# Kernel tuning notes

Hardware: AMD Instinct MI355X
Metric: run time of the kernel (lower is better)

Reference implementation:

```python
import jax, jax.numpy as jnp
import numpy as np
from jax import lax

B, FCH, H, W = 2, 48, 512, 512
WNUM, PATCH = 1, 8
DEG = 180.0 / np.pi
# well-conditioned, slightly asymmetric fallback Mueller matrix for masked (non-physical) pixels
_SAFE = np.array([[1.0, 0.02, 0.01, 0.005],
                  [0.0, 0.95, 0.05, 0.0],
                  [0.0, -0.05, 0.90, 0.04],
                  [0.0, 0.0, -0.04, 0.85]], dtype=np.float32)


def setup_inputs():
    key = jax.random.key(0)
    x = 0.5 * jax.random.normal(key, (B, FCH, H, W), dtype=jnp.float32)
    eye = jnp.eye(4, dtype=jnp.float32).reshape(16)
    # bias intensity frames and both calibration matrices toward 2*I so per-pixel
    # 4x4 systems are well conditioned and M is near-physical
    boost = jnp.concatenate([2.0 * eye, 2.0 * eye, 2.0 * eye])[None, :, None, None]
    return {"x": x + boost}


def _charpoly_mask(M):
    # Cloude realizability test: characteristic-polynomial coefficients of the
    # Hermitian coherency matrix must all be >= 0 (all eigenvalues >= 0).
    s = jnp.stack([jnp.eye(2, dtype=jnp.complex64),
                   jnp.array([[1, 0], [0, -1]], jnp.complex64),
                   jnp.array([[0, 1], [1, 0]], jnp.complex64),
                   jnp.array([[0, -1j], [1j, 0]], jnp.complex64)])
    Bk = jnp.einsum('iab,jcd->ijacbd', s, s).reshape(16, 4, 4)  # kron(sigma_i, sigma_j)
    Hc = 0.25 * jnp.einsum('...k,kab->...ab', M.reshape(M.shape[:-2] + (16,)).astype(jnp.complex64), Bk)
    tr1 = jnp.trace(Hc, axis1=-2, axis2=-1).real
    H2 = Hc @ Hc
    tr2 = jnp.trace(H2, axis1=-2, axis2=-1).real
    tr3 = jnp.trace(H2 @ Hc, axis1=-2, axis2=-1).real
    c2 = 0.5 * (tr1 ** 2 - tr2)
    c3 = (tr1 ** 3 - 3.0 * tr1 * tr2 + 2.0 * tr3) / 6.0
    c4 = jnp.linalg.det(Hc).real
    return (tr1 >= 0) & (c2 >= 0) & (c3 >= 0) & (c4 >= 0)


def _compute_mm(A, F, Wm, norm=True):
    M = jnp.linalg.solve(A, F)  # A^-1 F
    M = jnp.swapaxes(jnp.linalg.solve(jnp.swapaxes(Wm, -1, -2), jnp.swapaxes(M, -1, -2)), -1, -2)  # ... W^-1
    return M / M[..., 0:1, 0:1] if norm else M


def _lu_chipman(M, mask):
    # Lu-Chipman polar decomposition M = M_delta @ M_R @ M_D (per pixel)
    M = jnp.where(mask[..., None, None], M, jnp.asarray(_SAFE))
    I3 = jnp.eye(3, dtype=M.dtype)
    D = M[..., 0, 1:]  # diattenuation vector
    d2 = jnp.clip(jnp.sum(D * D, -1), 0.0, 1.0 - 1e-6)
    d = jnp.sqrt(d2 + 1e-12)
    sq = jnp.sqrt(1.0 - d2)
    Dh = D / jnp.maximum(d, 1e-6)[..., None]
    mD = sq[..., None, None] * I3 + (1.0 - sq)[..., None, None] * (Dh[..., :, None] * Dh[..., None, :])
    ones = jnp.ones(M.shape[:-2] + (1,), M.dtype)
    MD = jnp.concatenate([jnp.concatenate([ones, D], -1)[..., None, :],
                          jnp.concatenate([D[..., None], mD], -1)], -2)
    Mp = jnp.swapaxes(jnp.linalg.solve(MD, jnp.swapaxes(M, -1, -2)), -1, -2)  # M @ MD^-1 (MD symmetric)
    mp = Mp[..., 1:, 1:]
    mm = mp @ jnp.swapaxes(mp, -1, -2)
    lam = jnp.clip(jnp.linalg.eigvalsh(mm), 1e-12, None)  # ascending
    s1, s2, s3 = jnp.sqrt(lam[..., 2]), jnp.sqrt(lam[..., 1]), jnp.sqrt(lam[..., 0])
    sgn = jnp.where(jnp.linalg.det(mp) < 0, -1.0, 1.0).astype(M.dtype)
    A3 = mm + (s1 * s2 + s2 * s3 + s3 * s1)[..., None, None] * I3 + 1e-6 * I3
    B3 = (s1 + s2 + s3)[..., None, None] * mm + (s1 * s2 * s3)[..., None, None] * I3
    mdel = sgn[..., None, None] * jnp.linalg.solve(A3, B3)
    Pdel = (M[..., 1:, 0] - jnp.einsum('...ij,...j->...i', M[..., 1:, 1:], D)) / (1.0 - d2)[..., None]
    top = jnp.concatenate([ones, jnp.zeros(M.shape[:-2] + (3,), M.dtype)], -1)[..., None, :]
    Mdel = jnp.concatenate([top, jnp.concatenate([Pdel[..., None], mdel], -1)], -2)
    MR = jnp.linalg.solve(Mdel + 1e-6 * jnp.eye(4, dtype=M.dtype), Mp)
    return MD, MR, Mdel


def _polarimetry(MD, MR, Mdel):
    clipc = lambda t: jnp.clip(t, -1.0 + 1e-6, 1.0 - 1e-6)
    D = MD[..., 0, 1:]
    totD = jnp.sqrt(jnp.sum(D * D, -1) + 1e-12)
    linD = jnp.sqrt(D[..., 0] ** 2 + D[..., 1] ** 2 + 1e-12)
    cirD = jnp.abs(D[..., 2])
    totR = jnp.arccos(clipc(jnp.trace(MR, axis1=-2, axis2=-1) / 2.0 - 1.0)) * DEG
    mR = MR[..., 1:, 1:]
    linR = jnp.arccos(clipc(jnp.sqrt((mR[..., 0, 0] + mR[..., 1, 1]) ** 2
                                     + (mR[..., 1, 0] - mR[..., 0, 1]) ** 2 + 1e-12) - 1.0)) * DEG
    cirR = 0.5 * jnp.arctan2(mR[..., 1, 0] - mR[..., 0, 1], mR[..., 0, 0] + mR[..., 1, 1]) * DEG
    # azimuth of linear retardance from retardance-vector components (r1, r2)
    azi = jnp.mod(0.5 * jnp.arctan2(mR[..., 2, 0] - mR[..., 0, 2], mR[..., 1, 2] - mR[..., 2, 1]) * DEG, 180.0)
    dazi = jnp.mod(0.5 * jnp.arctan2(D[..., 1], D[..., 0]) * DEG, 180.0)
    totP = 1.0 - jnp.abs(jnp.trace(Mdel[..., 1:, 1:], axis1=-2, axis2=-1)) / 3.0
    # p[:,0]=diattenuation, p[:,6]=linear retardance, p[:,7]=azimuth, p[:,-1]=depolarization
    return jnp.stack([totD, linD, cirD, totR, cirR, dazi, linR, azi, totP], axis=1)


def _rolling_circstd(a_deg, patch):
    # circstd(a/180*pi, high=pi, low=0) over patch x patch sliding windows, back to degrees.
    # circstd reduces to window means of cos/sin of doubled angles -> avg pooling.
    th = a_deg * (2.0 * np.pi / 180.0)
    wsum = lambda t: lax.reduce_window(t, 0.0, lax.add, (1, 1, patch, patch), (1, 1, 1, 1), 'SAME')
    cnt = wsum(jnp.ones_like(a_deg))
    R = jnp.sqrt(wsum(jnp.cos(th)) ** 2 + wsum(jnp.sin(th)) ** 2 + 1e-12) / cnt
    R = jnp.clip(R, 1e-7, 1.0 - 1e-7)
    return 0.5 * jnp.sqrt(-2.0 * jnp.log(R)) * DEG


def _forward(x):
    b, f, h, w = x.shape
    xw = jnp.moveaxis(x.reshape(b, WNUM, f // WNUM, h, w), 2, -1)  # (b, wnum, h, w, 48)
    Fi = xw[..., :16].reshape(b, WNUM, h, w, 4, 4)
    Am = xw[..., 16:32].reshape(b, WNUM, h, w, 4, 4)
    Wm = xw[..., 32:48].reshape(b, WNUM, h, w, 4, 4)
    M = _compute_mm(Am, Fi, Wm, norm=True)
    inten = xw[..., 0]
    imin = inten.min(axis=(1, 2, 3), keepdims=True)
    imax = inten.max(axis=(1, 2, 3), keepdims=True)
    inorm = (inten - imin) / (imax - imin)
    mchan = jnp.moveaxis(M.reshape(b, WNUM, h, w, 16), -1, 2).reshape(b, WNUM * 16, h, w)
    v = lax.stop_gradient(_charpoly_mask(M))
    MD, MR, Mdel = _lu_chipman(M, v)
    p = _polarimetry(MD, MR, Mdel)  # (b, 9, wnum, h, w)
    std = _rolling_circstd(p[:, 7], PATCH)
    # concat order matches forward: intensity, mueller, linr, totp, datt, azimuth, std
    return jnp.concatenate([inorm, mchan, p[:, 6], p[:, 8], p[:, 0], p[:, 7], std], axis=1)


def reference(x):
    return _forward(x)
```

## Files before the change

kernel.cpp:

```cpp
#include <hip/hip_runtime.h>
#include <math.h>

#define B_ 2
#define H_ 512
#define W_ 512
#define HW_ (H_ * W_)
#define NCH_IN 48
#define NCH_OUT 22

__device__ __forceinline__ unsigned int fkey(float f) {
    unsigned int u = __float_as_uint(f);
    return (u & 0x80000000u) ? ~u : (u | 0x80000000u);
}
__device__ __forceinline__ float funkey(unsigned int k) {
    return (k & 0x80000000u) ? __uint_as_float(k ^ 0x80000000u) : __uint_as_float(~k);
}

__global__ void init_mm_kernel(unsigned int* mm) {
    mm[0] = 0xFFFFFFFFu; mm[1] = 0u;
    mm[2] = 0xFFFFFFFFu; mm[3] = 0u;
}

__global__ __launch_bounds__(256) void minmax_kernel(const float* __restrict__ x,
                                                     unsigned int* __restrict__ mm) {
    int b = blockIdx.x >> 6;
    int blk = blockIdx.x & 63;
    const float* src = x + (size_t)b * NCH_IN * HW_;
    float lo = INFINITY, hi = -INFINITY;
    for (int i = blk * 256 + threadIdx.x; i < HW_; i += 64 * 256) {
        float v = src[i];
        lo = fminf(lo, v);
        hi = fmaxf(hi, v);
    }
    __shared__ float slo[256], shi[256];
    slo[threadIdx.x] = lo; shi[threadIdx.x] = hi;
    __syncthreads();
    for (int s = 128; s > 0; s >>= 1) {
        if (threadIdx.x < s) {
            slo[threadIdx.x] = fminf(slo[threadIdx.x], slo[threadIdx.x + s]);
            shi[threadIdx.x] = fmaxf(shi[threadIdx.x], shi[threadIdx.x + s]);
        }
        __syncthreads();
    }
    if (threadIdx.x == 0) {
        atomicMin(&mm[2 * b], fkey(slo[0]));
        atomicMax(&mm[2 * b + 1], fkey(shi[0]));
    }
}

__device__ __forceinline__ void inv4(const float A[4][4], float out[4][4]) {
    float m[4][8];
#pragma unroll
    for (int i = 0; i < 4; i++) {
#pragma unroll
        for (int j = 0; j < 4; j++) {
            m[i][j] = A[i][j];
            m[i][j + 4] = (i == j) ? 1.0f : 0.0f;
        }
    }
#pragma unroll
    for (int k = 0; k < 4; k++) {
#pragma unroll
        for (int r = k + 1; r < 4; r++) {
            bool sw = fabsf(m[r][k]) > fabsf(m[k][k]);
#pragma unroll
            for (int c = 0; c < 8; c++) {
                float a = m[k][c], b = m[r][c];
                m[k][c] = sw ? b : a;
                m[r][c] = sw ? a : b;
            }
        }
        float piv = 1.0f / m[k][k];
#pragma unroll
        for (int c = 0; c < 8; c++) m[k][c] *= piv;
#pragma unroll
        for (int r = 0; r < 4; r++) {
            if (r == k) continue;
            float f = m[r][k];
#pragma unroll
            for (int c = 0; c < 8; c++) m[r][c] -= f * m[k][c];
        }
    }
#pragma unroll
    for (int i = 0; i < 4; i++)
#pragma unroll
        for (int j = 0; j < 4; j++) out[i][j] = m[i][j + 4];
}

__device__ __forceinline__ void mul4(const float A[4][4], const float B[4][4], float C[4][4]) {
#pragma unroll
    for (int i = 0; i < 4; i++)
#pragma unroll
        for (int j = 0; j < 4; j++) {
            float s = 0.0f;
#pragma unroll
            for (int k = 0; k < 4; k++) s += A[i][k] * B[k][j];
            C[i][j] = s;
        }
}

__device__ __forceinline__ void inv3(const float A[3][3], float out[3][3]) {
    float c00 = A[1][1] * A[2][2] - A[1][2] * A[2][1];
    float c01 = A[1][2] * A[2][0] - A[1][0] * A[2][2];
    float c02 = A[1][0] * A[2][1] - A[1][1] * A[2][0];
    float det = A[0][0] * c00 + A[0][1] * c01 + A[0][2] * c02;
    float id = 1.0f / det;
    out[0][0] = c00 * id;
    out[0][1] = (A[0][2] * A[2][1] - A[0][1] * A[2][2]) * id;
    out[0][2] = (A[0][1] * A[1][2] - A[0][2] * A[1][1]) * id;
    out[1][0] = c01 * id;
    out[1][1] = (A[0][0] * A[2][2] - A[0][2] * A[2][0]) * id;
    out[1][2] = (A[0][2] * A[1][0] - A[0][0] * A[1][2]) * id;
    out[2][0] = c02 * id;
    out[2][1] = (A[0][1] * A[2][0] - A[0][0] * A[2][1]) * id;
    out[2][2] = (A[0][0] * A[1][1] - A[0][1] * A[1][0]) * id;
}

__device__ __forceinline__ float det3(const float A[3][3]) {
    return A[0][0] * (A[1][1] * A[2][2] - A[1][2] * A[2][1])
         - A[0][1] * (A[1][0] * A[2][2] - A[1][2] * A[2][0])
         + A[0][2] * (A[1][0] * A[2][1] - A[1][1] * A[2][0]);
}

__device__ __forceinline__ void eig3_sym(const float A[3][3], float& l1, float& l2, float& l3) {
    float q = (A[0][0] + A[1][1] + A[2][2]) * (1.0f / 3.0f);
    float a00 = A[0][0] - q, a11 = A[1][1] - q, a22 = A[2][2] - q;
    float off = A[0][1] * A[0][1] + A[0][2] * A[0][2] + A[1][2] * A[1][2];
    float p2 = a00 * a00 + a11 * a11 + a22 * a22 + 2.0f * off;
    float p = sqrtf(p2 * (1.0f / 6.0f) + 1e-30f);
    float inv = 1.0f / p;
    float b00 = a00 * inv, b11 = a11 * inv, b22 = a22 * inv;
    float b01 = A[0][1] * inv, b02 = A[0][2] * inv, b12 = A[1][2] * inv;
    float detB = b00 * (b11 * b22 - b12 * b12)
               - b01 * (b01 * b22 - b12 * b02)
               + b02 * (b01 * b12 - b11 * b02);
    float r = 0.5f * detB;
    r = fminf(fmaxf(r, -1.0f), 1.0f);
    float phi = acosf(r) * (1.0f / 3.0f);
    l1 = q + 2.0f * p * cosf(phi);
    l3 = q + 2.0f * p * cosf(phi + 2.0943951023931953f);
    l2 = 3.0f * q - l1 - l3;
}

#define DEG_ 57.29577951308232f

__global__ __launch_bounds__(256) void main_kernel(const float* __restrict__ x,
                                                   const unsigned int* __restrict__ mmk,
                                                   float* __restrict__ out) {
    int idx = blockIdx.x * 256 + threadIdx.x;
    if (idx >= B_ * HW_) return;
    int b = idx / HW_;
    int p = idx - b * HW_;
    const float* src = x + (size_t)b * NCH_IN * HW_ + p;

    float F[4][4], A[4][4], Wm[4][4];
#pragma unroll
    for (int i = 0; i < 4; i++)
#pragma unroll
        for (int j = 0; j < 4; j++) {
            F[i][j]  = src[(4 * i + j) * HW_];
            A[i][j]  = src[(16 + 4 * i + j) * HW_];
            Wm[i][j] = src[(32 + 4 * i + j) * HW_];
        }
    float inten = F[0][0];

    float Ai[4][4], Wi[4][4], T[4][4], M[4][4];
    inv4(A, Ai);
    mul4(Ai, F, T);
    inv4(Wm, Wi);
    mul4(T, Wi, M);
    float nrm = 1.0f / M[0][0];
#pragma unroll
    for (int i = 0; i < 4; i++)
#pragma unroll
        for (int j = 0; j < 4; j++) M[i][j] *= nrm;

    float* ob = out + (size_t)b * NCH_OUT * HW_ + p;
    float imin = funkey(mmk[2 * b]), imax = funkey(mmk[2 * b + 1]);
    ob[0] = (inten - imin) / (imax - imin);
#pragma unroll
    for (int k = 0; k < 16; k++) ob[(size_t)(1 + k) * HW_] = M[k >> 2][k & 3];

    float Vr[4][4], Vi[4][4];
#pragma unroll
    for (int i = 0; i < 4; i++) {
        Vr[i][0] = M[i][0] + M[i][1]; Vi[i][0] = 0.0f;
        Vr[i][1] = M[i][0] - M[i][1]; Vi[i][1] = 0.0f;
        Vr[i][2] = M[i][2];           Vi[i][2] = -M[i][3];
        Vr[i][3] = M[i][2];           Vi[i][3] =  M[i][3];
    }
    float Hr[4][4], Hi[4][4];
    {
        const int cc[4] = {0, 1, 0, 1};
        const int dd[4] = {0, 1, 1, 0};
#pragma unroll
        for (int t = 0; t < 4; t++) {
            float wr = Vr[0][t] + Vr[1][t], wi = Vi[0][t] + Vi[1][t];
            float xr = Vr[0][t] - Vr[1][t], xi = Vi[0][t] - Vi[1][t];
            float yr = Vr[2][t] + Vi[3][t], yi = Vi[2][t] - Vr[3][t];
            float zr = Vr[2][t] - Vi[3][t], zi = Vi[2][t] + Vr[3][t];
            int c = cc[t], d = dd[t];
            Hr[c][d]         = 0.25f * wr; Hi[c][d]         = 0.25f * wi;
            Hr[c][2 + d]     = 0.25f * yr; Hi[c][2 + d]     = 0.25f * yi;
            Hr[2 + c][d]     = 0.25f * zr; Hi[2 + c][d]     = 0.25f * zi;
            Hr[2 + c][2 + d] = 0.25f * xr; Hi[2 + c][2 + d] = 0.25f * xi;
        }
    }
    float H2r[4][4], H2i[4][4];
#pragma unroll
    for (int i = 0; i < 4; i++)
#pragma unroll
        for (int j = 0; j < 4; j++) {
            float sr = 0.0f, si = 0.0f;
#pragma unroll
            for (int k = 0; k < 4; k++) {
                sr += Hr[i][k] * Hr[k][j] - Hi[i][k] * Hi[k][j];
                si += Hr[i][k] * Hi[k][j] + Hi[i][k] * Hr[k][j];
            }
            H2r[i][j] = sr; H2i[i][j] = si;
        }
    float tr1 = Hr[0][0] + Hr[1][1] + Hr[2][2] + Hr[3][3];
    float p2t = H2r[0][0] + H2r[1][1] + H2r[2][2] + H2r[3][3];
    float p3t = 0.0f, p4t = 0.0f;
#pragma unroll
    for (int i = 0; i < 4; i++)
#pragma unroll
        for (int j = 0; j < 4; j++) {
            p3t += H2r[i][j] * Hr[i][j] + H2i[i][j] * Hi[i][j];
            p4t += H2r[i][j] * H2r[i][j] + H2i[i][j] * H2i[i][j];
        }
    float c2 = 0.5f * (tr1 * tr1 - p2t);
    float c3 = (tr1 * tr1 * tr1 - 3.0f * tr1 * p2t + 2.0f * p3t) * (1.0f / 6.0f);
    float c4 = (tr1 * tr1 * tr1 * tr1 - 6.0f * tr1 * tr1 * p2t + 3.0f * p2t * p2t
                + 8.0f * tr1 * p3t - 6.0f * p4t) * (1.0f / 24.0f);
    bool mask = (tr1 >= 0.0f) && (c2 >= 0.0f) && (c3 >= 0.0f) && (c4 >= 0.0f);

    const float SAFE[4][4] = {{1.0f, 0.02f, 0.01f, 0.005f},
                              {0.0f, 0.95f, 0.05f, 0.0f},
                              {0.0f, -0.05f, 0.9f, 0.04f},
                              {0.0f, 0.0f, -0.04f, 0.85f}};
#pragma unroll
    for (int i = 0; i < 4; i++)
#pragma unroll
        for (int j = 0; j < 4; j++) M[i][j] = mask ? M[i][j] : SAFE[i][j];

    float D0 = M[0][1], D1 = M[0][2], D2v = M[0][3];
    float d2 = D0 * D0 + D1 * D1 + D2v * D2v;
    float totD = sqrtf(d2 + 1e-12f);
    d2 = fminf(fmaxf(d2, 0.0f), 1.0f - 1e-6f);
    float d = sqrtf(d2 + 1e-12f);
    float sq = sqrtf(1.0f - d2);
    float dinv = 1.0f / fmaxf(d, 1e-6f);
    float h0 = D0 * dinv, h1 = D1 * dinv, h2 = D2v * dinv;
    float omsq = 1.0f - sq;
    float MD[4][4];
    MD[0][0] = 1.0f; MD[0][1] = D0; MD[0][2] = D1; MD[0][3] = D2v;
    MD[1][0] = D0; MD[2][0] = D1; MD[3][0] = D2v;
    MD[1][1] = sq + omsq * h0 * h0; MD[1][2] = omsq * h0 * h1; MD[1][3] = omsq * h0 * h2;
    MD[2][1] = MD[1][2]; MD[2][2] = sq + omsq * h1 * h1; MD[2][3] = omsq * h1 * h2;
    MD[3][1] = MD[1][3]; MD[3][2] = MD[2][3]; MD[3][3] = sq + omsq * h2 * h2;

    float MDi[4][4], Mp[4][4];
    inv4(MD, MDi);
    mul4(M, MDi, Mp);

    float mp3[3][3];
#pragma unroll
    for (int i = 0; i < 3; i++)
#pragma unroll
        for (int j = 0; j < 3; j++) mp3[i][j] = Mp[1 + i][1 + j];
    float mmS[3][3];
#pragma unroll
    for (int i = 0; i < 3; i++)
#pragma unroll
        for (int j = 0; j < 3; j++) {
            float s = 0.0f;
#pragma unroll
            for (int k = 0; k < 3; k++) s += mp3[i][k] * mp3[j][k];
            mmS[i][j] = s;
        }
    float l1, l2, l3;
    eig3_sym(mmS, l1, l2, l3);
    l1 = fmaxf(l1, 1e-12f); l2 = fmaxf(l2, 1e-12f); l3 = fmaxf(l3, 1e-12f);
    float s1 = sqrtf(l1), s2 = sqrtf(l2), s3 = sqrtf(l3);
    float sgn = (det3(mp3) < 0.0f) ? -1.0f : 1.0f;

    float e2s = s1 * s2 + s2 * s3 + s3 * s1 + 1e-6f;
    float e1s = s1 + s2 + s3;
    float e3s = s1 * s2 * s3;
    float A3[3][3], B3[3][3];
#pragma unroll
    for (int i = 0; i < 3; i++)
#pragma unroll
        for (int j = 0; j < 3; j++) {
            A3[i][j] = mmS[i][j] + ((i == j) ? e2s : 0.0f);
            B3[i][j] = e1s * mmS[i][j] + ((i == j) ? e3s : 0.0f);
        }
    float A3i[3][3];
    inv3(A3, A3i);
    float mdel[3][3];
#pragma unroll
    for (int i = 0; i < 3; i++)
#pragma unroll
        for (int j = 0; j < 3; j++) {
            float s = 0.0f;
#pragma unroll
            for (int k = 0; k < 3; k++) s += A3i[i][k] * B3[k][j];
            mdel[i][j] = sgn * s;
        }

    float inv1md2 = 1.0f / (1.0f - d2);
    float Pd[3];
#pragma unroll
    for (int i = 0; i < 3; i++)
        Pd[i] = (M[1 + i][0] - (M[1 + i][1] * D0 + M[1 + i][2] * D1 + M[1 + i][3] * D2v)) * inv1md2;

    float a_eps = 1.0f + 1e-6f;
    float MR0[4];
#pragma unroll
    for (int j = 0; j < 4; j++) MR0[j] = Mp[0][j] / a_eps;
    float m3[3][3];
#pragma unroll
    for (int i = 0; i < 3; i++)
#pragma unroll
        for (int j = 0; j < 3; j++) m3[i][j] = mdel[i][j] + ((i == j) ? 1e-6f : 0.0f);
    float m3i[3][3];
    inv3(m3, m3i);
    float MRr[3][4];
#pragma unroll
    for (int i = 0; i < 3; i++)
#pragma unroll
        for (int j = 0; j < 4; j++) {
            float s = 0.0f;
#pragma unroll
            for (int k = 0; k < 3; k++) s += m3i[i][k] * (Mp[1 + k][j] - Pd[k] * MR0[j]);
            MRr[i][j] = s;
        }

    float mR00 = MRr[0][1], mR01 = MRr[0][2], mR02 = MRr[0][3];
    float mR10 = MRr[1][1], mR11 = MRr[1][2], mR12 = MRr[1][3];
    float mR20 = MRr[2][1], mR21 = MRr[2][2];

    float t_lin = sqrtf((mR00 + mR11) * (mR00 + mR11) + (mR10 - mR01) * (mR10 - mR01) + 1e-12f) - 1.0f;
    t_lin = fminf(fmaxf(t_lin, -1.0f + 1e-6f), 1.0f - 1e-6f);
    float linR = acosf(t_lin) * DEG_;

    float azi = 0.5f * atan2f(mR20 - mR02, mR12 - mR21) * DEG_;
    azi = fmodf(azi, 180.0f);
    if (azi < 0.0f) azi += 180.0f;

    float totP = 1.0f - fabsf(mdel[0][0] + mdel[1][1] + mdel[2][2]) * (1.0f / 3.0f);

    ob[(size_t)17 * HW_] = linR;
    ob[(size_t)18 * HW_] = totP;
    ob[(size_t)19 * HW_] = totD;
    ob[(size_t)20 * HW_] = azi;
}

__global__ __launch_bounds__(256) void hpass_kernel(const float* __restrict__ out,
                                                    float* __restrict__ hc,
                                                    float* __restrict__ hs) {
    int gid = blockIdx.x;
    int tile = gid & 1;
    int rowg = gid >> 1;
    int b = rowg / H_;
    int y = rowg - b * H_;
    const float* azi = out + (size_t)b * NCH_OUT * HW_ + (size_t)20 * HW_ + (size_t)y * W_;
    __shared__ float lc[263], ls[263];
    int tx = tile * 256;
    for (int i = threadIdx.x; i < 263; i += 256) {
        int gx = tx - 3 + i;
        float c = 0.0f, s = 0.0f;
        if (gx >= 0 && gx < W_) {
            float th = azi[gx] * 0.03490658503988659f;
            __sincosf(th, &s, &c);
        }
        lc[i] = c; ls[i] = s;
    }
    __syncthreads();
    float sc = 0.0f, ss = 0.0f;
#pragma unroll
    for (int d = 0; d < 8; d++) {
        sc += lc[threadIdx.x + d];
        ss += ls[threadIdx.x + d];
    }
    int o = (b * H_ + y) * W_ + tx + threadIdx.x;
    hc[o] = sc;
    hs[o] = ss;
}

__global__ __launch_bounds__(256) void vpass_kernel(const float* __restrict__ hc,
                                                    const float* __restrict__ hs,
                                                    float* __restrict__ out) {
    int idx = blockIdx.x * 256 + threadIdx.x;
    if (idx >= B_ * HW_) return;
    int b = idx / HW_;
    int p = idx - b * HW_;
    int y = p / W_;
    int xc = p - y * W_;
    float sc = 0.0f, ss = 0.0f;
#pragma unroll
    for (int dy = -3; dy <= 4; dy++) {
        int yy = y + dy;
        if (yy >= 0 && yy < H_) {
            int o = b * HW_ + yy * W_ + xc;
            sc += hc[o];
            ss += hs[o];
        }
    }
    float rows = (float)(min(y + 5, H_) - max(y - 3, 0));
    float cols = (float)(min(xc + 5, W_) - max(xc - 3, 0));
    float cnt = rows * cols;
    float R = sqrtf(sc * sc + ss * ss + 1e-12f) / cnt;
    R = fminf(fmaxf(R, 1e-7f), 1.0f - 1e-7f);
    float stdv = 0.5f * sqrtf(-2.0f * logf(R)) * DEG_;
    out[(size_t)b * NCH_OUT * HW_ + (size_t)21 * HW_ + p] = stdv;
}

extern "C" void kernel_launch(void* const* d_in, const int* in_sizes, int n_in,
                              void* d_out, int out_size, void* d_ws, size_t ws_size,
                              hipStream_t stream) {
    const float* x = (const float*)d_in[0];
    float* out = (float*)d_out;
    unsigned int* mmk = (unsigned int*)d_ws;
    float* hc = (float*)d_ws + 16;
    float* hs = hc + (size_t)B_ * HW_;

    hipLaunchKernelGGL(init_mm_kernel, dim3(1), dim3(1), 0, stream, mmk);
    hipLaunchKernelGGL(minmax_kernel, dim3(128), dim3(256), 0, stream, x, mmk);
    hipLaunchKernelGGL(main_kernel, dim3((B_ * HW_ + 255) / 256), dim3(256), 0, stream, x, mmk, out);
    hipLaunchKernelGGL(hpass_kernel, dim3(B_ * H_ * (W_ / 256)), dim3(256), 0, stream, out, hc, hs);
    hipLaunchKernelGGL(vpass_kernel, dim3((B_ * HW_ + 255) / 256), dim3(256), 0, stream, hc, hs, out);
}
```

Baseline: 187.3 us.

## Use direct solves, closed-form MD inverse, fast math, and fused tiled circular std

Replaces the explicit 4x4 inversions with Gauss-Jordan solves on augmented matrices. Swaps the generic inversion of the diattenuation matrix for its closed-form inverse. Switches to hardware rcp/sqrt intrinsics and polynomial acos/atan2 approximations, and drops the now-redundant fmod. Fuses the separate horizontal and vertical circular-std passes into one 2D-tiled shared-memory kernel, removing a workspace round trip and a launch. The approximations reduce accuracy and could push outputs near the tolerance, and the tiled kernel recomputes sin/cos for halo pixels.

```diff
diff --git a/kernel.cpp b/kernel.cpp
--- a/kernel.cpp
+++ b/kernel.cpp
@@ -7,6 +7,29 @@
 #define HW_ (H_ * W_)
 #define NCH_IN 48
 #define NCH_OUT 22
+#define DEG_ 57.29577951308232f
+
+__device__ __forceinline__ float frcp(float x)  { return __builtin_amdgcn_rcpf(x); }
+__device__ __forceinline__ float fsqrtf_(float x){ return __builtin_amdgcn_sqrtf(x); }
+
+__device__ __forceinline__ float fast_acos(float x) {
+    float ax = fabsf(x);
+    float t = fsqrtf_(fmaxf(1.0f - ax, 0.0f));
+    float p = t * (1.5707288f + ax * (-0.2121144f + ax * (0.0742610f + ax * (-0.0187293f))));
+    return (x >= 0.0f) ? p : (3.14159265358979f - p);
+}
+
+__device__ __forceinline__ float fast_atan2(float y, float x) {
+    float ay = fabsf(y), ax = fabsf(x);
+    float mx = fmaxf(ax, ay), mn = fminf(ax, ay);
+    float a = mn * frcp(fmaxf(mx, 1e-37f));
+    float s = a * a;
+    float r = a * (0.99997726f + s * (-0.33262347f + s * (0.19354346f +
+              s * (-0.11643287f + s * (0.05265332f + s * (-0.01172120f))))));
+    if (ay > ax) r = 1.57079632679f - r;
+    if (x < 0.0f) r = 3.14159265359f - r;
+    return (y < 0.0f) ? -r : r;
+}
 
 __device__ __forceinline__ unsigned int fkey(float f) {
     unsigned int u = __float_as_uint(f);
@@ -48,15 +71,12 @@
     }
 }
 
-__device__ __forceinline__ void inv4(const float A[4][4], float out[4][4]) {
+__device__ __forceinline__ void solve4(const float A[4][4], const float Bm[4][4], float X[4][4]) {
     float m[4][8];
 #pragma unroll
     for (int i = 0; i < 4; i++) {
 #pragma unroll
-        for (int j = 0; j < 4; j++) {
-            m[i][j] = A[i][j];
-            m[i][j + 4] = (i == j) ? 1.0f : 0.0f;
-        }
+        for (int j = 0; j < 4; j++) { m[i][j] = A[i][j]; m[i][j + 4] = Bm[i][j]; }
     }
 #pragma unroll
     for (int k = 0; k < 4; k++) {
@@ -70,7 +90,7 @@
                 m[r][c] = sw ? a : b;
             }
         }
-        float piv = 1.0f / m[k][k];
+        float piv = frcp(m[k][k]);
 #pragma unroll
         for (int c = 0; c < 8; c++) m[k][c] *= piv;
 #pragma unroll
@@ -84,7 +104,7 @@
 #pragma unroll
     for (int i = 0; i < 4; i++)
 #pragma unroll
-        for (int j = 0; j < 4; j++) out[i][j] = m[i][j + 4];
+        for (int j = 0; j < 4; j++) X[i][j] = m[i][j + 4];
 }
 
 __device__ __forceinline__ void mul4(const float A[4][4], const float B[4][4], float C[4][4]) {
@@ -104,7 +124,7 @@
     float c01 = A[1][2] * A[2][0] - A[1][0] * A[2][2];
     float c02 = A[1][0] * A[2][1] - A[1][1] * A[2][0];
     float det = A[0][0] * c00 + A[0][1] * c01 + A[0][2] * c02;
-    float id = 1.0f / det;
+    float id = frcp(det);
     out[0][0] = c00 * id;
     out[0][1] = (A[0][2] * A[2][1] - A[0][1] * A[2][2]) * id;
     out[0][2] = (A[0][1] * A[1][2] - A[0][2] * A[1][1]) * id;
@@ -127,8 +147,8 @@
     float a00 = A[0][0] - q, a11 = A[1][1] - q, a22 = A[2][2] - q;
     float off = A[0][1] * A[0][1] + A[0][2] * A[0][2] + A[1][2] * A[1][2];
     float p2 = a00 * a00 + a11 * a11 + a22 * a22 + 2.0f * off;
-    float p = sqrtf(p2 * (1.0f / 6.0f) + 1e-30f);
-    float inv = 1.0f / p;
+    float p = fsqrtf_(p2 * (1.0f / 6.0f) + 1e-30f);
+    float inv = frcp(p);
     float b00 = a00 * inv, b11 = a11 * inv, b22 = a22 * inv;
     float b01 = A[0][1] * inv, b02 = A[0][2] * inv, b12 = A[1][2] * inv;
     float detB = b00 * (b11 * b22 - b12 * b12)
@@ -136,13 +156,11 @@
                + b02 * (b01 * b12 - b11 * b02);
     float r = 0.5f * detB;
     r = fminf(fmaxf(r, -1.0f), 1.0f);
-    float phi = acosf(r) * (1.0f / 3.0f);
-    l1 = q + 2.0f * p * cosf(phi);
-    l3 = q + 2.0f * p * cosf(phi + 2.0943951023931953f);
+    float phi = fast_acos(r) * (1.0f / 3.0f);
+    l1 = q + 2.0f * p * __cosf(phi);
+    l3 = q + 2.0f * p * __cosf(phi + 2.0943951023931953f);
     l2 = 3.0f * q - l1 - l3;
 }
-
-#define DEG_ 57.29577951308232f
 
 __global__ __launch_bounds__(256) void main_kernel(const float* __restrict__ x,
                                                    const unsigned int* __restrict__ mmk,
@@ -153,31 +171,33 @@
     int p = idx - b * HW_;
     const float* src = x + (size_t)b * NCH_IN * HW_ + p;
 
-    float F[4][4], A[4][4], Wm[4][4];
+    float F[4][4], A[4][4], WT[4][4];
 #pragma unroll
     for (int i = 0; i < 4; i++)
 #pragma unroll
         for (int j = 0; j < 4; j++) {
             F[i][j]  = src[(4 * i + j) * HW_];
             A[i][j]  = src[(16 + 4 * i + j) * HW_];
-            Wm[i][j] = src[(32 + 4 * i + j) * HW_];
+            WT[j][i] = src[(32 + 4 * i + j) * HW_];
         }
     float inten = F[0][0];
 
-    float Ai[4][4], Wi[4][4], T[4][4], M[4][4];
-    inv4(A, Ai);
-    mul4(Ai, F, T);
-    inv4(Wm, Wi);
-    mul4(T, Wi, M);
-    float nrm = 1.0f / M[0][0];
-#pragma unroll
-    for (int i = 0; i < 4; i++)
-#pragma unroll
-        for (int j = 0; j < 4; j++) M[i][j] *= nrm;
+    float X[4][4], XT[4][4], MT[4][4], M[4][4];
+    solve4(A, F, X);
+#pragma unroll
+    for (int i = 0; i < 4; i++)
+#pragma unroll
+        for (int j = 0; j < 4; j++) XT[i][j] = X[j][i];
+    solve4(WT, XT, MT);
+    float nrm = frcp(MT[0][0]);
+#pragma unroll
+    for (int i = 0; i < 4; i++)
+#pragma unroll
+        for (int j = 0; j < 4; j++) M[i][j] = MT[j][i] * nrm;
 
     float* ob = out + (size_t)b * NCH_OUT * HW_ + p;
     float imin = funkey(mmk[2 * b]), imax = funkey(mmk[2 * b + 1]);
-    ob[0] = (inten - imin) / (imax - imin);
+    ob[0] = (inten - imin) * frcp(imax - imin);
 #pragma unroll
     for (int k = 0; k < 16; k++) ob[(size_t)(1 + k) * HW_] = M[k >> 2][k & 3];
 
@@ -245,23 +265,30 @@
         for (int j = 0; j < 4; j++) M[i][j] = mask ? M[i][j] : SAFE[i][j];
 
     float D0 = M[0][1], D1 = M[0][2], D2v = M[0][3];
-    float d2 = D0 * D0 + D1 * D1 + D2v * D2v;
-    float totD = sqrtf(d2 + 1e-12f);
-    d2 = fminf(fmaxf(d2, 0.0f), 1.0f - 1e-6f);
-    float d = sqrtf(d2 + 1e-12f);
-    float sq = sqrtf(1.0f - d2);
-    float dinv = 1.0f / fmaxf(d, 1e-6f);
+    float d2r = D0 * D0 + D1 * D1 + D2v * D2v;
+    float totD = fsqrtf_(d2r + 1e-12f);
+    float d2 = fminf(fmaxf(d2r, 0.0f), 1.0f - 1e-6f);
+    float d = fsqrtf_(d2 + 1e-12f);
+    float sq2 = 1.0f - d2;
+    float sq = fsqrtf_(sq2);
+    float dinv = frcp(fmaxf(d, 1e-6f));
     float h0 = D0 * dinv, h1 = D1 * dinv, h2 = D2v * dinv;
-    float omsq = 1.0f - sq;
-    float MD[4][4];
-    MD[0][0] = 1.0f; MD[0][1] = D0; MD[0][2] = D1; MD[0][3] = D2v;
-    MD[1][0] = D0; MD[2][0] = D1; MD[3][0] = D2v;
-    MD[1][1] = sq + omsq * h0 * h0; MD[1][2] = omsq * h0 * h1; MD[1][3] = omsq * h0 * h2;
-    MD[2][1] = MD[1][2]; MD[2][2] = sq + omsq * h1 * h1; MD[2][3] = omsq * h1 * h2;
-    MD[3][1] = MD[1][3]; MD[3][2] = MD[2][3]; MD[3][3] = sq + omsq * h2 * h2;
-
-    float MDi[4][4], Mp[4][4];
-    inv4(MD, MDi);
+
+    float isq2 = frcp(sq2);
+    float isq = frcp(sq);
+    float cdh = (1.0f - sq) * isq2;
+    float MDi[4][4];
+    MDi[0][0] = isq2;
+    MDi[0][1] = -isq2 * D0; MDi[0][2] = -isq2 * D1; MDi[0][3] = -isq2 * D2v;
+    MDi[1][0] = MDi[0][1];  MDi[2][0] = MDi[0][2];  MDi[3][0] = MDi[0][3];
+    float Dh[3] = {h0, h1, h2};
+#pragma unroll
+    for (int i = 0; i < 3; i++)
+#pragma unroll
+        for (int j = 0; j < 3; j++)
+            MDi[1 + i][1 + j] = ((i == j) ? isq : 0.0f) + cdh * Dh[i] * Dh[j];
+
+    float Mp[4][4];
     mul4(M, MDi, Mp);
 
     float mp3[3][3];
@@ -282,7 +309,7 @@
     float l1, l2, l3;
     eig3_sym(mmS, l1, l2, l3);
     l1 = fmaxf(l1, 1e-12f); l2 = fmaxf(l2, 1e-12f); l3 = fmaxf(l3, 1e-12f);
-    float s1 = sqrtf(l1), s2 = sqrtf(l2), s3 = sqrtf(l3);
+    float s1 = fsqrtf_(l1), s2 = fsqrtf_(l2), s3 = fsqrtf_(l3);
     float sgn = (det3(mp3) < 0.0f) ? -1.0f : 1.0f;
 
     float e2s = s1 * s2 + s2 * s3 + s3 * s1 + 1e-6f;
@@ -309,16 +336,15 @@
             mdel[i][j] = sgn * s;
         }
 
-    float inv1md2 = 1.0f / (1.0f - d2);
     float Pd[3];
 #pragma unroll
     for (int i = 0; i < 3; i++)
-        Pd[i] = (M[1 + i][0] - (M[1 + i][1] * D0 + M[1 + i][2] * D1 + M[1 + i][3] * D2v)) * inv1md2;
-
-    float a_eps = 1.0f + 1e-6f;
+        Pd[i] = (M[1 + i][0] - (M[1 + i][1] * D0 + M[1 + i][2] * D1 + M[1 + i][3] * D2v)) * isq2;
+
     float MR0[4];
-#pragma unroll
-    for (int j = 0; j < 4; j++) MR0[j] = Mp[0][j] / a_eps;
+    const float inv_aeps = 1.0f / (1.0f + 1e-6f);
+#pragma unroll
+    for (int j = 0; j < 4; j++) MR0[j] = Mp[0][j] * inv_aeps;
     float m3[3][3];
 #pragma unroll
     for (int i = 0; i < 3; i++)
@@ -341,12 +367,11 @@
     float mR10 = MRr[1][1], mR11 = MRr[1][2], mR12 = MRr[1][3];
     float mR20 = MRr[2][1], mR21 = MRr[2][2];
 
-    float t_lin = sqrtf((mR00 + mR11) * (mR00 + mR11) + (mR10 - mR01) * (mR10 - mR01) + 1e-12f) - 1.0f;
+    float t_lin = fsqrtf_((mR00 + mR11) * (mR00 + mR11) + (mR10 - mR01) * (mR10 - mR01) + 1e-12f) - 1.0f;
     t_lin = fminf(fmaxf(t_lin, -1.0f + 1e-6f), 1.0f - 1e-6f);
-    float linR = acosf(t_lin) * DEG_;
-
-    float azi = 0.5f * atan2f(mR20 - mR02, mR12 - mR21) * DEG_;
-    azi = fmodf(azi, 180.0f);
+    float linR = fast_acos(t_lin) * DEG_;
+
+    float azi = 0.5f * fast_atan2(mR20 - mR02, mR12 - mR21) * DEG_;
     if (azi < 0.0f) azi += 180.0f;
 
     float totP = 1.0f - fabsf(mdel[0][0] + mdel[1][1] + mdel[2][2]) * (1.0f / 3.0f);
@@ -357,64 +382,55 @@
     ob[(size_t)20 * HW_] = azi;
 }
 
-__global__ __launch_bounds__(256) void hpass_kernel(const float* __restrict__ out,
-                                                    float* __restrict__ hc,
-                                                    float* __restrict__ hs) {
-    int gid = blockIdx.x;
-    int tile = gid & 1;
-    int rowg = gid >> 1;
-    int b = rowg / H_;
-    int y = rowg - b * H_;
-    const float* azi = out + (size_t)b * NCH_OUT * HW_ + (size_t)20 * HW_ + (size_t)y * W_;
-    __shared__ float lc[263], ls[263];
-    int tx = tile * 256;
-    for (int i = threadIdx.x; i < 263; i += 256) {
-        int gx = tx - 3 + i;
+#define TX_ 32
+#define TY_ 8
+__global__ __launch_bounds__(256) void circstd_kernel(float* __restrict__ out) {
+    int tx0 = blockIdx.x * TX_;
+    int ty0 = blockIdx.y * TY_;
+    int b = blockIdx.z;
+    const float* azi = out + (size_t)b * NCH_OUT * HW_ + (size_t)20 * HW_;
+
+    __shared__ float lc[TY_ + 7][TX_ + 8];
+    __shared__ float ls[TY_ + 7][TX_ + 8];
+    __shared__ float hc[TY_ + 7][TX_];
+    __shared__ float hs[TY_ + 7][TX_];
+
+    for (int i = threadIdx.x; i < (TY_ + 7) * (TX_ + 7); i += 256) {
+        int row = i / (TX_ + 7);
+        int col = i - row * (TX_ + 7);
+        int gy = ty0 - 3 + row;
+        int gx = tx0 - 3 + col;
         float c = 0.0f, s = 0.0f;
-        if (gx >= 0 && gx < W_) {
-            float th = azi[gx] * 0.03490658503988659f;
+        if (gy >= 0 && gy < H_ && gx >= 0 && gx < W_) {
+            float th = azi[(size_t)gy * W_ + gx] * 0.03490658503988659f;
             __sincosf(th, &s, &c);
         }
-        lc[i] = c; ls[i] = s;
+        lc[row][col] = c; ls[row][col] = s;
     }
     __syncthreads();
+
+    for (int i = threadIdx.x; i < (TY_ + 7) * TX_; i += 256) {
+        int row = i / TX_;
+        int col = i - row * TX_;
+        float sc = 0.0f, ss = 0.0f;
+#pragma unroll
+        for (int d = 0; d < 8; d++) { sc += lc[row][col + d]; ss += ls[row][col + d]; }
+        hc[row][col] = sc; hs[row][col] = ss;
+    }
+    __syncthreads();
+
+    int col = threadIdx.x & (TX_ - 1);
+    int row = threadIdx.x >> 5;
     float sc = 0.0f, ss = 0.0f;
 #pragma unroll
-    for (int d = 0; d < 8; d++) {
-        sc += lc[threadIdx.x + d];
-        ss += ls[threadIdx.x + d];
-    }
-    int o = (b * H_ + y) * W_ + tx + threadIdx.x;
-    hc[o] = sc;
-    hs[o] = ss;
-}
-
-__global__ __launch_bounds__(256) void vpass_kernel(const float* __restrict__ hc,
-                                                    const float* __restrict__ hs,
-                                                    float* __restrict__ out) {
-    int idx = blockIdx.x * 256 + threadIdx.x;
-    if (idx >= B_ * HW_) return;
-    int b = idx / HW_;
-    int p = idx - b * HW_;
-    int y = p / W_;
-    int xc = p - y * W_;
-    float sc = 0.0f, ss = 0.0f;
-#pragma unroll
-    for (int dy = -3; dy <= 4; dy++) {
-        int yy = y + dy;
-        if (yy >= 0 && yy < H_) {
-            int o = b * HW_ + yy * W_ + xc;
-            sc += hc[o];
-            ss += hs[o];
-        }
-    }
+    for (int k = 0; k < 8; k++) { sc += hc[row + k][col]; ss += hs[row + k][col]; }
+    int y = ty0 + row, xc = tx0 + col;
     float rows = (float)(min(y + 5, H_) - max(y - 3, 0));
     float cols = (float)(min(xc + 5, W_) - max(xc - 3, 0));
-    float cnt = rows * cols;
-    float R = sqrtf(sc * sc + ss * ss + 1e-12f) / cnt;
+    float R = fsqrtf_(sc * sc + ss * ss + 1e-12f) * frcp(rows * cols);
     R = fminf(fmaxf(R, 1e-7f), 1.0f - 1e-7f);
-    float stdv = 0.5f * sqrtf(-2.0f * logf(R)) * DEG_;
-    out[(size_t)b * NCH_OUT * HW_ + (size_t)21 * HW_ + p] = stdv;
+    float stdv = 0.5f * fsqrtf_(-2.0f * __logf(R)) * DEG_;
+    out[(size_t)b * NCH_OUT * HW_ + (size_t)21 * HW_ + (size_t)y * W_ + xc] = stdv;
 }
 
 extern "C" void kernel_launch(void* const* d_in, const int* in_sizes, int n_in,
@@ -423,12 +439,9 @@
     const float* x = (const float*)d_in[0];
     float* out = (float*)d_out;
     unsigned int* mmk = (unsigned int*)d_ws;
-    float* hc = (float*)d_ws + 16;
-    float* hs = hc + (size_t)B_ * HW_;
 
     hipLaunchKernelGGL(init_mm_kernel, dim3(1), dim3(1), 0, stream, mmk);
     hipLaunchKernelGGL(minmax_kernel, dim3(128), dim3(256), 0, stream, x, mmk);
     hipLaunchKernelGGL(main_kernel, dim3((B_ * HW_ + 255) / 256), dim3(256), 0, stream, x, mmk, out);
-    hipLaunchKernelGGL(hpass_kernel, dim3(B_ * H_ * (W_ / 256)), dim3(256), 0, stream, out, hc, hs);
-    hipLaunchKernelGGL(vpass_kernel, dim3((B_ * HW_ + 255) / 256), dim3(256), 0, stream, hc, hs, out);
-}
+    hipLaunchKernelGGL(circstd_kernel, dim3(W_ / TX_, H_ / TY_, B_), dim3(256), 0, stream, out);
+}
```

Result: faster. 177.6 us (-5.2%).
